# Kernel optimization log

Measured on AMD Instinct MI355X. Metric: run time of the kernel, lower is better.

## Reference

```python
import jax, jax.numpy as jnp
import numpy as np

K = 2      # kernelsize
S = 2      # stride
FM = 32    # featuremaps


def extract_patches(x, k, s):
    """Mimic tf.image.extract_patches VALID: depth ordered (ki, kj, c)."""
    B, H, W, C = x.shape
    oh = (H - k) // s + 1
    ow = (W - k) // s + 1
    # k*k strided slices, each [B, oh, ow, C]; stacked -> [B, oh, ow, kk, C]
    cols = [x[:, i:i + s * oh:s, j:j + s * ow:s, :]
            for i in range(k) for j in range(k)]
    p = jnp.stack(cols, axis=3)
    return p.reshape(B, oh, ow, k * k * C)  # depth layout (ki, kj, c)


def setup_inputs() -> dict:
    key = jax.random.key(0)
    kx, k1, k2 = jax.random.split(key, 3)
    B, H, W, C = 8, 64, 64, 16
    kk = K * K
    x = jax.random.normal(kx, (B, H, W, C), dtype=jnp.float32)
    # VarianceScaling(2.0, untruncated_normal): std = sqrt(2/fan_in)
    W1 = jax.random.normal(k1, (C, kk, FM), dtype=jnp.float32) * np.sqrt(2.0 / kk)
    W2 = jax.random.normal(k2, (C, kk * kk, FM), dtype=jnp.float32) * np.sqrt(2.0 / (kk * kk))
    return {"x": x, "W1": W1, "W2": W2}


def reference(x, W1, W2):
    B, H, W_, C = x.shape
    kk = K * K
    pv = extract_patches(x, K, S)                 # [B, oh, ow, kk*C]
    oh, ow = pv.shape[1], pv.shape[2]
    # Faithful to source: raw reshape (NOT transpose) of (kk*C) -> (C, kk),
    # reinterpreting the (ki,kj,c)-ordered depth as rows of length kk.
    p = pv.reshape(B, oh, ow, C, kk)
    # tf.linalg.matmul([C,kk], [C,kk,F]) broadcasts -> z1[c,a,f] = sum_m p[a,m] W1[c,m,f]
    z1 = jnp.einsum('bhwam,cmf->bhwcaf', p, W1)
    # second-order outer product per row: [C, kk, kk] -> [C, kk*kk]
    so = (p[..., :, None] * p[..., None, :]).reshape(B, oh, ow, C, kk * kk)
    z2 = jnp.einsum('bhwaq,cqf->bhwcaf', so, W2)
    # per-patch [C, C, F] flattened to C*C*F channels, matching the source reshape
    return (z1 + z2).reshape(B, oh, ow, C * C * FM)
```

## Files before the change

kernel.cpp:

```cpp
#include <hip/hip_runtime.h>


typedef float f4 __attribute__((ext_vector_type(4)));

#define LPB 4

__global__ __launch_bounds__(256) void quad_kernel(
    const float* __restrict__ x,
    const float* __restrict__ W1,
    const float* __restrict__ W2,
    float* __restrict__ out)
{
    __shared__ __align__(16) float p_lds[64];
    __shared__ __align__(16) float so_lds[256];

    const int t  = threadIdx.x;
    const int f4off = (t & 7) * 4;
    const int s  = t >> 3;
    const int c  = s & 15;
    const int a0 = (s >> 4) * 8;

    f4 w1r[4];
    f4 w2r[16];
    {
        const float* W1p = W1 + c * 128 + f4off;
#pragma unroll
        for (int m = 0; m < 4; ++m)
            w1r[m] = *(const f4*)(W1p + m * 32);
        const float* W2p = W2 + c * 512 + f4off;
#pragma unroll
        for (int q = 0; q < 16; ++q)
            w2r[q] = *(const f4*)(W2p + q * 32);
    }

    const int loc0 = blockIdx.x * LPB;

    for (int i = 0; i < LPB; ++i) {
        const int loc = loc0 + i;
        const int b  = loc >> 10;
        const int hw = loc & 1023;
        const int h  = hw >> 5;
        const int w  = hw & 31;

        __syncthreads();
        if (t < 16) {
            const int quad = t >> 2;
            const int ki = quad >> 1, kj = quad & 1;
            const int l4 = (t & 3) * 4;
            const float* src =
                x + (((b * 64 + 2 * h + ki) * 64) + 2 * w + kj) * 16 + l4;
            *(f4*)&p_lds[quad * 16 + l4] = *(const f4*)src;
        }
        __syncthreads();
        {
            const int a = t >> 4, q = t & 15;
            so_lds[t] = p_lds[a * 4 + (q >> 2)] * p_lds[a * 4 + (q & 3)];
        }
        __syncthreads();

        float* outp = out + (size_t)loc * 8192 + c * 512 + f4off;

#pragma unroll
        for (int j = 0; j < 8; ++j) {
            const int a = a0 + j;
            const f4 pv  = *(const f4*)&p_lds[a * 4];
            const f4 so0 = *(const f4*)&so_lds[a * 16];
            const f4 so1 = *(const f4*)&so_lds[a * 16 + 4];
            const f4 so2 = *(const f4*)&so_lds[a * 16 + 8];
            const f4 so3 = *(const f4*)&so_lds[a * 16 + 12];

            f4 acc = (f4)0.0f;
            acc += pv.x  * w1r[0];
            acc += pv.y  * w1r[1];
            acc += pv.z  * w1r[2];
            acc += pv.w  * w1r[3];
            acc += so0.x * w2r[0];
            acc += so0.y * w2r[1];
            acc += so0.z * w2r[2];
            acc += so0.w * w2r[3];
            acc += so1.x * w2r[4];
            acc += so1.y * w2r[5];
            acc += so1.z * w2r[6];
            acc += so1.w * w2r[7];
            acc += so2.x * w2r[8];
            acc += so2.y * w2r[9];
            acc += so2.z * w2r[10];
            acc += so2.w * w2r[11];
            acc += so3.x * w2r[12];
            acc += so3.y * w2r[13];
            acc += so3.z * w2r[14];
            acc += so3.w * w2r[15];

            __builtin_nontemporal_store(acc, (f4*)(outp + a * 32));
        }
    }
}

extern "C" void kernel_launch(void* const* d_in, const int* in_sizes, int n_in,
                              void* d_out, int out_size, void* d_ws, size_t ws_size,
                              hipStream_t stream) {
    const float* x  = (const float*)d_in[0];
    const float* W1 = (const float*)d_in[1];
    const float* W2 = (const float*)d_in[2];
    float* out = (float*)d_out;

    const int n_loc = 8 * 32 * 32;
    dim3 grid(n_loc / LPB), block(256);
    quad_kernel<<<grid, block, 0, stream>>>(x, W1, W2, out);
}
```

Baseline: 278.8 us.

## Factor quadratic form per row and load patches directly into registers

Removes the shared-memory staging of patch values and outer products, along with its three block barriers. Each thread now loads its 8 patch rows straight from global memory into registers. The second-order term is factored as p^T(W1 + W2·p), which needs fewer multiply-adds than forming the outer product. A minimum-occupancy hint is added to launch bounds; the risks are redundant global loads across threads and changed floating-point summation order.

```diff
diff --git a/kernel.cpp b/kernel.cpp
--- a/kernel.cpp
+++ b/kernel.cpp
@@ -5,20 +5,17 @@
 
 #define LPB 4
 
-__global__ __launch_bounds__(256) void quad_kernel(
+__global__ __launch_bounds__(256, 3) void quad_kernel(
     const float* __restrict__ x,
     const float* __restrict__ W1,
     const float* __restrict__ W2,
     float* __restrict__ out)
 {
-    __shared__ __align__(16) float p_lds[64];
-    __shared__ __align__(16) float so_lds[256];
-
-    const int t  = threadIdx.x;
+    const int t     = threadIdx.x;
     const int f4off = (t & 7) * 4;
-    const int s  = t >> 3;
-    const int c  = s & 15;
-    const int a0 = (s >> 4) * 8;
+    const int s     = t >> 3;
+    const int c     = s & 15;
+    const int half  = s >> 4;
 
     f4 w1r[4];
     f4 w2r[16];
@@ -42,56 +39,46 @@
         const int h  = hw >> 5;
         const int w  = hw & 31;
 
-        __syncthreads();
-        if (t < 16) {
-            const int quad = t >> 2;
-            const int ki = quad >> 1, kj = quad & 1;
-            const int l4 = (t & 3) * 4;
-            const float* src =
-                x + (((b * 64 + 2 * h + ki) * 64) + 2 * w + kj) * 16 + l4;
-            *(f4*)&p_lds[quad * 16 + l4] = *(const f4*)src;
-        }
-        __syncthreads();
-        {
-            const int a = t >> 4, q = t & 15;
-            so_lds[t] = p_lds[a * 4 + (q >> 2)] * p_lds[a * 4 + (q & 3)];
-        }
-        __syncthreads();
+        const float* src =
+            x + (((b * 64 + 2 * h + half) * 64) + 2 * w) * 16;
+        f4 pv[8];
+#pragma unroll
+        for (int j = 0; j < 8; ++j)
+            pv[j] = *(const f4*)(src + j * 4);
 
-        float* outp = out + (size_t)loc * 8192 + c * 512 + f4off;
+        float* outp = out + (size_t)loc * 8192 + c * 512 + half * 256 + f4off;
 
 #pragma unroll
         for (int j = 0; j < 8; ++j) {
-            const int a = a0 + j;
-            const f4 pv  = *(const f4*)&p_lds[a * 4];
-            const f4 so0 = *(const f4*)&so_lds[a * 16];
-            const f4 so1 = *(const f4*)&so_lds[a * 16 + 4];
-            const f4 so2 = *(const f4*)&so_lds[a * 16 + 8];
-            const f4 so3 = *(const f4*)&so_lds[a * 16 + 12];
+            const f4 P = pv[j];
 
-            f4 acc = (f4)0.0f;
-            acc += pv.x  * w1r[0];
-            acc += pv.y  * w1r[1];
-            acc += pv.z  * w1r[2];
-            acc += pv.w  * w1r[3];
-            acc += so0.x * w2r[0];
-            acc += so0.y * w2r[1];
-            acc += so0.z * w2r[2];
-            acc += so0.w * w2r[3];
-            acc += so1.x * w2r[4];
-            acc += so1.y * w2r[5];
-            acc += so1.z * w2r[6];
-            acc += so1.w * w2r[7];
-            acc += so2.x * w2r[8];
-            acc += so2.y * w2r[9];
-            acc += so2.z * w2r[10];
-            acc += so2.w * w2r[11];
-            acc += so3.x * w2r[12];
-            acc += so3.y * w2r[13];
-            acc += so3.z * w2r[14];
-            acc += so3.w * w2r[15];
+            f4 t0 = w1r[0];
+            f4 t1 = w1r[1];
+            f4 t2 = w1r[2];
+            f4 t3 = w1r[3];
+            t0 += P.x * w2r[0];
+            t1 += P.x * w2r[4];
+            t2 += P.x * w2r[8];
+            t3 += P.x * w2r[12];
+            t0 += P.y * w2r[1];
+            t1 += P.y * w2r[5];
+            t2 += P.y * w2r[9];
+            t3 += P.y * w2r[13];
+            t0 += P.z * w2r[2];
+            t1 += P.z * w2r[6];
+            t2 += P.z * w2r[10];
+            t3 += P.z * w2r[14];
+            t0 += P.w * w2r[3];
+            t1 += P.w * w2r[7];
+            t2 += P.w * w2r[11];
+            t3 += P.w * w2r[15];
 
-            __builtin_nontemporal_store(acc, (f4*)(outp + a * 32));
+            f4 acc = P.x * t0;
+            acc += P.y * t1;
+            acc += P.z * t2;
+            acc += P.w * t3;
+
+            __builtin_nontemporal_store(acc, (f4*)(outp + j * 32));
         }
     }
 }
```

Measured after the change: 282.4 us. Within noise of the previous version (+1.3%).
